# Kernel optimization log

Hardware: AMD Instinct MI355X
Metric: run time of the kernel (lower is better)

## Reference

```python
import jax, jax.numpy as jnp
import numpy as np
import math

V, TB, C, H, L = 50257, 1024, 1024, 16, 8
B, T = 2, 1024
D = C // H


def setup_inputs() -> dict:
    key = jax.random.key(0)
    ks = jax.random.split(key, 16)
    s = 0.02
    n = lambda k, shp: (jax.random.normal(k, shp, jnp.float32) * s)
    inp = {
        "idx": jax.random.randint(ks[0], (B, T), 0, V),
        "tok_emb": n(ks[1], (V, C)),
        "pos_emb": n(ks[2], (1, TB, C)),
        # per-layer stacked params (torch Linear convention: W is [out, in])
        "Wq": n(ks[3], (L, C, C)), "bq": jnp.zeros((L, C)),
        "Wk": n(ks[4], (L, C, C)), "bk": jnp.zeros((L, C)),
        "Wv": n(ks[5], (L, C, C)), "bv": jnp.zeros((L, C)),
        "Wp": n(ks[6], (L, C, C)), "bp": jnp.zeros((L, C)),
        "ln1_w": jnp.ones((L, C)), "ln1_b": jnp.zeros((L, C)),
        "ln2_w": jnp.ones((L, C)), "ln2_b": jnp.zeros((L, C)),
        "W1": n(ks[7], (L, 4 * C, C)), "b1": jnp.zeros((L, 4 * C)),
        "W2": n(ks[8], (L, C, 4 * C)), "b2": jnp.zeros((L, C)),
        "lnf_w": jnp.ones((C,)), "lnf_b": jnp.zeros((C,)),
        "head_w": n(ks[9], (V, C)),
    }
    return inp


def _layer_norm(x, w, b, eps=1e-5):
    mu = x.mean(-1, keepdims=True)
    var = x.var(-1, keepdims=True)
    return (x - mu) * jax.lax.rsqrt(var + eps) * w + b


def _gpt_forward(idx, tok_emb, pos_emb, Wq, bq, Wk, bk, Wv, bv, Wp, bp,
                 ln1_w, ln1_b, ln2_w, ln2_b, W1, b1, W2, b2, lnf_w, lnf_b, head_w):
    b, t = idx.shape
    x = tok_emb[idx] + pos_emb[:, :t, :]  # [B, T, C]; drop = identity (eval)
    causal = jnp.tril(jnp.ones((t, t), dtype=bool))  # [T, T]
    scale = 1.0 / math.sqrt(D)

    def block(x, p):
        (wq, bq_, wk, bk_, wv, bv_, wp, bp_, l1w, l1b, l2w, l2b, w1, b1_, w2, b2_) = p
        h = _layer_norm(x, l1w, l1b)
        q = (h @ wq.T + bq_).reshape(b, t, H, D).transpose(0, 2, 1, 3)  # [B,H,T,D]
        k = (h @ wk.T + bk_).reshape(b, t, H, D).transpose(0, 2, 1, 3)
        v = (h @ wv.T + bv_).reshape(b, t, H, D).transpose(0, 2, 1, 3)
        att = jnp.einsum("bhqd,bhkd->bhqk", q, k) * scale
        att = jnp.where(causal, att, -jnp.inf)
        att = jax.nn.softmax(att, axis=-1)
        y = jnp.einsum("bhqk,bhkd->bhqd", att, v)
        y = y.transpose(0, 2, 1, 3).reshape(b, t, C)
        x = x + (y @ wp.T + bp_)
        h2 = _layer_norm(x, l2w, l2b)
        m = jax.nn.gelu(h2 @ w1.T + b1_, approximate=False)  # torch nn.GELU (erf)
        x = x + (m @ w2.T + b2_)
        return x, None

    params = (Wq, bq, Wk, bk, Wv, bv, Wp, bp, ln1_w, ln1_b, ln2_w, ln2_b, W1, b1, W2, b2)
    x, _ = jax.lax.scan(block, x, params)
    x = _layer_norm(x, lnf_w, lnf_b)
    logits = x @ head_w.T  # [B, T, V]
    return logits


def reference(idx, tok_emb, pos_emb, Wq, bq, Wk, bk, Wv, bv, Wp, bp,
              ln1_w, ln1_b, ln2_w, ln2_b, W1, b1, W2, b2, lnf_w, lnf_b, head_w):
    return _gpt_forward(idx, tok_emb, pos_emb, Wq, bq, Wk, bk, Wv, bv, Wp, bp,
                        ln1_w, ln1_b, ln2_w, ln2_b, W1, b1, W2, b2, lnf_w, lnf_b, head_w)
```

## Files before the change

kernel.cpp:

```cpp
#include <hip/hip_runtime.h>
#include <math.h>

#define V_ 50257
#define C_ 1024
#define H_ 16
#define L_ 8
#define B_ 2
#define T_ 1024
#define BT_ 2048
#define CC_ (C_*C_)
#define QLD_ 3072

typedef unsigned short ushort_t;
using bf16x8 = __attribute__((ext_vector_type(8))) short;
using f32x4  = __attribute__((ext_vector_type(4))) float;

#define AS1 __attribute__((address_space(1)))
#define AS3 __attribute__((address_space(3)))
#define VMCNT0() asm volatile("s_waitcnt vmcnt(0)" ::: "memory")
#define LGKM0()  asm volatile("s_waitcnt lgkmcnt(0)" ::: "memory")
#define RBAR()   asm volatile("s_barrier" ::: "memory")

__device__ __forceinline__ ushort_t f2bf(float f){
  union { float f; unsigned u; } a; a.f = f;
  unsigned r = a.u + 0x7fffu + ((a.u >> 16) & 1u);
  return (ushort_t)(r >> 16);
}

__device__ __forceinline__ unsigned cvtpk_bf16(float a, float b){
  unsigned r;
  asm("v_cvt_pk_bf16_f32 %0, %1, %2" : "=v"(r) : "v"(a), "v"(b));
  return r;
}

__device__ __forceinline__ float wave_sum(float v){
  #pragma unroll
  for(int o=32;o>0;o>>=1) v += __shfl_down(v,o,64);
  return v;
}

__global__ __launch_bounds__(256) void cvt_blk(const float* __restrict__ s, ushort_t* __restrict__ d,
    long inner4, int nblk, long dstStride4){
  long total = inner4 * nblk;
  for(long i = (long)blockIdx.x*256 + threadIdx.x; i < total; i += (long)gridDim.x*256){
    long blk = i / inner4, r = i - blk*inner4;
    float4 v = ((const float4*)s)[i];
    ushort4 o; o.x=f2bf(v.x); o.y=f2bf(v.y); o.z=f2bf(v.z); o.w=f2bf(v.w);
    ((ushort4*)d)[blk*dstStride4 + r] = o;
  }
}

__global__ __launch_bounds__(256) void pack_qkv_bias(const float* __restrict__ bq,
    const float* __restrict__ bk, const float* __restrict__ bv, float* __restrict__ dst){
  int i = blockIdx.x*256 + threadIdx.x;
  int l = i / QLD_, c = i - l*QLD_;
  float v;
  if(c < C_)            v = bq[l*C_ + c];
  else if(c < 2*C_)     v = bk[l*C_ + c - C_];
  else                  v = bv[l*C_ + c - 2*C_];
  dst[i] = v;
}

__global__ __launch_bounds__(256) void embed_kernel(const int* __restrict__ idx,
    const float* __restrict__ tok, const float* __restrict__ pos, float* __restrict__ x){
  int i = blockIdx.x*256 + threadIdx.x;
  int c = i & (C_-1); int bt = i >> 10; int t = bt & (T_-1);
  x[i] = tok[(size_t)idx[bt]*C_ + c] + pos[t*C_ + c];
}

__global__ __launch_bounds__(256) void ln_kernel(const float* in, const float* __restrict__ w,
    const float* __restrict__ b, float* outF, ushort_t* outB){
  int row = blockIdx.x;
  const float* xr = in + (size_t)row*C_;
  float vals[4]; float sum=0.f, sq=0.f;
  #pragma unroll
  for(int l=0;l<4;l++){ float v = xr[threadIdx.x + l*256]; vals[l]=v; sum+=v; sq+=v*v; }
  __shared__ float r1[4], r2[4];
  float s1 = wave_sum(sum), s2 = wave_sum(sq);
  int wid = threadIdx.x>>6, lane = threadIdx.x&63;
  if(lane==0){ r1[wid]=s1; r2[wid]=s2; }
  __syncthreads();
  float tot  = r1[0]+r1[1]+r1[2]+r1[3];
  float tot2 = r2[0]+r2[1]+r2[2]+r2[3];
  float mu  = tot * (1.f/C_);
  float var = tot2 * (1.f/C_) - mu*mu;
  float inv = rsqrtf(var + 1e-5f);
  #pragma unroll
  for(int l=0;l<4;l++){
    int c = threadIdx.x + l*256;
    float v = (vals[l]-mu)*inv*w[c] + b[c];
    if(outB) outB[(size_t)row*C_ + c] = f2bf(v);
    else     outF[(size_t)row*C_ + c] = v;
  }
}

template<int BN>
__global__ __launch_bounds__(256) void gemm_mfma(
    const ushort_t* __restrict__ A, const ushort_t* __restrict__ W,
    const float* __restrict__ bias, const float* resid,
    float* outF, ushort_t* outB,
    int M, int N, int K, int act, int nt, int qs)
{
  constexpr int BM = 128;
  constexpr int NSB = BN/16;
  constexpr int NBF = BN/32;
  __shared__ __align__(16) short sA[3][8*512];
  __shared__ __align__(16) short sB[3][NSB*512];
  const int tid  = threadIdx.x;
  const int lane = tid & 63, wid = tid >> 6;
  const int wr = wid >> 1, wc = wid & 1;
  const int nwg = gridDim.x * gridDim.y;
  const int lid = blockIdx.x + gridDim.x * blockIdx.y;
  const int swz = (lid & 7) * (nwg >> 3) + (lid >> 3);
  const int m0 = (swz % gridDim.x) * BM, n0 = (swz / gridDim.x) * BN;
  const int r16 = lane & 15, kq = lane >> 4;

  auto stage = [&](int buf, int k0){
    #pragma unroll
    for(int s2=0; s2<2; ++s2){
      int s = wid*2 + s2;
      const ushort_t* g = A + (size_t)(m0 + s*16 + r16)*K + k0 + kq*8;
      __builtin_amdgcn_global_load_lds((const AS1 void*)g,
          (AS3 void*)&sA[buf][s*512], 16, 0, 0);
    }
    #pragma unroll
    for(int s2=0; s2<NSB/4; ++s2){
      int s = wid*(NSB/4) + s2;
      int gn = n0 + s*16 + r16; if(gn >= N) gn = N-1;
      const ushort_t* g = W + (size_t)gn*K + k0 + kq*8;
      __builtin_amdgcn_global_load_lds((const AS1 void*)g,
          (AS3 void*)&sB[buf][s*512], 16, 0, 0);
    }
  };

  f32x4 acc[4][NBF];
  #pragma unroll
  for(int i=0;i<4;i++)
    #pragma unroll
    for(int j=0;j<NBF;j++) acc[i][j] = (f32x4){0.f,0.f,0.f,0.f};

  const int NT = K >> 5;
  stage(0, 0); stage(1, 32); stage(2, 64);

  int cur = 0;
  for(int t=0; t<NT; ++t){
    if(t+2 < NT){
      if constexpr(BN==128) asm volatile("s_waitcnt vmcnt(8)" ::: "memory");
      else                  asm volatile("s_waitcnt vmcnt(6)" ::: "memory");
    } else if(t+1 < NT){
      if constexpr(BN==128) asm volatile("s_waitcnt vmcnt(4)" ::: "memory");
      else                  asm volatile("s_waitcnt vmcnt(3)" ::: "memory");
    } else {
      VMCNT0();
    }
    RBAR();
    bf16x8 af[4], bfr[NBF];
    #pragma unroll
    for(int m=0;m<4;m++) af[m] = *(const bf16x8*)&sA[cur][(wr*4+m)*512 + lane*8];
    #pragma unroll
    for(int n=0;n<NBF;n++) bfr[n] = *(const bf16x8*)&sB[cur][(wc*NBF+n)*512 + lane*8];
    LGKM0();
    RBAR();
    if(t+3 < NT) stage(cur, (t+3)*32);
    #pragma unroll
    for(int m=0;m<4;m++)
      #pragma unroll
      for(int n=0;n<NBF;n++)
        acc[m][n] = __builtin_amdgcn_mfma_f32_16x16x32_bf16(af[m], bfr[n], acc[m][n], 0, 0, 0);
    cur = (cur==2) ? 0 : cur+1;
  }

  const int colb = n0 + wc*(BN/2);
  #pragma unroll
  for(int m=0;m<4;m++){
    int rowb = m0 + wr*64 + m*16 + kq*4;
    #pragma unroll
    for(int n=0;n<NBF;n++){
      int col = colb + n*16 + r16;
      if(col >= N) continue;
      float bv = bias ? bias[col] : 0.f;
      #pragma unroll
      for(int i=0;i<4;i++){
        int row = rowb + i;
        float v = acc[m][n][i] + bv;
        if(qs && col < C_) v *= 0.125f;
        if(act) v = 0.5f*v*(1.f + erff(v*0.70710678118654752f));
        if(resid) v += resid[(size_t)row*N + col];
        if(outB) outB[(size_t)row*N + col] = f2bf(v);
        else if(nt) __builtin_nontemporal_store(v, &outF[(size_t)row*N + col]);
        else outF[(size_t)row*N + col] = v;
      }
    }
  }
}

__global__ __launch_bounds__(256) void flash_kernel(const ushort_t* __restrict__ qkv,
    ushort_t* __restrict__ y){
  const int tid = threadIdx.x, lane = tid & 63, wid = tid >> 6;
  const int r16 = lane & 15, kq = lane >> 4;
  const int lid = blockIdx.x + 16*blockIdx.y;
  const int swz = (lid & 7)*64 + (lid >> 3);
  const int qt = swz & 15, bh = swz >> 4;
  const int b = bh >> 4, h = bh & 15;
  const int q0 = qt*64, qw0 = q0 + wid*16;
  const int qa = qw0 + r16;

  __shared__ __align__(16) short Kt[2][8][512];
  __shared__ __align__(16) short VT[2][64][68];
  __shared__ __align__(16) short Pl[4][16][68];
  __shared__ __align__(16) short Ol[4][16][68];

  const size_t rowQ = (size_t)(b*T_ + qa)*QLD_ + h*64 + kq*8;
  bf16x8 qf0 = *(const bf16x8*)(qkv + rowQ);
  bf16x8 qf1 = *(const bf16x8*)(qkv + rowQ + 32);

  auto stageK = [&](int buf, int jt){
    #pragma unroll
    for(int s2=0;s2<2;s2++){
      int s = wid*2 + s2;
      const ushort_t* g = qkv + (size_t)(b*T_ + jt*64 + (s>>1)*16 + r16)*QLD_
                          + C_ + h*64 + (s&1)*32 + kq*8;
      __builtin_amdgcn_global_load_lds((const AS1 void*)g,
          (AS3 void*)&Kt[buf][s][lane*8], 16, 0, 0);
    }
  };

  f32x4 acc[4];
  #pragma unroll
  for(int t=0;t<4;t++) acc[t] = (f32x4){0.f,0.f,0.f,0.f};
  float m_r = -INFINITY, l_r = 0.f;

  {
    stageK(0, 0);
    const ushort_t* vg = qkv + (size_t)(b*T_ + lane)*QLD_ + 2*C_ + h*64;
    bf16x8 va = *(const bf16x8*)(vg + wid*8);
    bf16x8 vb = *(const bf16x8*)(vg + 32 + wid*8);
    VMCNT0();
    #pragma unroll
    for(int j=0;j<8;j++){ VT[0][wid*8+j][lane]=va[j]; VT[0][32+wid*8+j][lane]=vb[j]; }
    __syncthreads();
  }

  const int njt = qt + 1;
  for(int jt=0; jt<njt; ++jt){
    const int cur = jt & 1;
    const bool more = (jt+1) < njt;
    bf16x8 vr0, vr1;
    if(more){
      stageK(cur^1, jt+1);
      const ushort_t* vg = qkv + (size_t)(b*T_ + (jt+1)*64 + lane)*QLD_ + 2*C_ + h*64;
      vr0 = *(const bf16x8*)(vg + wid*8);
      vr1 = *(const bf16x8*)(vg + 32 + wid*8);
    }

    f32x4 st[4];
    __builtin_amdgcn_s_setprio(1);
    #pragma unroll
    for(int kr=0;kr<4;kr++){
      st[kr] = (f32x4){0.f,0.f,0.f,0.f};
      st[kr] = __builtin_amdgcn_mfma_f32_16x16x32_bf16(*(const bf16x8*)&Kt[cur][kr*2+0][lane*8], qf0, st[kr], 0,0,0);
      st[kr] = __builtin_amdgcn_mfma_f32_16x16x32_bf16(*(const bf16x8*)&Kt[cur][kr*2+1][lane*8], qf1, st[kr], 0,0,0);
    }
    __builtin_amdgcn_s_setprio(0);

    float vals[16];
    if(jt == njt-1){
      #pragma unroll
      for(int kr=0;kr<4;kr++)
        #pragma unroll
        for(int i=0;i<4;i++){
          int ka = jt*64 + kr*16 + 4*kq + i;
          vals[kr*4+i] = (ka <= qa) ? st[kr][i] : -INFINITY;
        }
    } else {
      #pragma unroll
      for(int kr=0;kr<4;kr++)
        #pragma unroll
        for(int i=0;i<4;i++) vals[kr*4+i] = st[kr][i];
    }
    float t8[8];
    #pragma unroll
    for(int i=0;i<8;i++) t8[i] = fmaxf(vals[i], vals[i+8]);
    float t4a = fmaxf(t8[0],t8[4]), t4b = fmaxf(t8[1],t8[5]);
    float t4c = fmaxf(t8[2],t8[6]), t4d = fmaxf(t8[3],t8[7]);
    float pmax = fmaxf(fmaxf(t4a,t4b), fmaxf(t4c,t4d));
    pmax = fmaxf(pmax, __shfl_xor(pmax, 16, 64));
    pmax = fmaxf(pmax, __shfl_xor(pmax, 32, 64));

    if(!__all(pmax - m_r <= 8.f)){
      float mnew = fmaxf(m_r, pmax);
      float alpha = __expf(m_r - mnew);
      l_r *= alpha;
      #pragma unroll
      for(int t=0;t<4;t++)
        #pragma unroll
        for(int j=0;j<4;j++) acc[t][j] *= alpha;
      m_r = mnew;
    }

    float ps = 0.f;
    #pragma unroll
    for(int kr=0;kr<4;kr++){
      float p0 = __expf(vals[kr*4+0]-m_r), p1 = __expf(vals[kr*4+1]-m_r);
      float p2 = __expf(vals[kr*4+2]-m_r), p3 = __expf(vals[kr*4+3]-m_r);
      ps += (p0+p1)+(p2+p3);
      *(unsigned*)&Pl[wid][r16][kr*16 + 4*kq]     = cvtpk_bf16(p0, p1);
      *(unsigned*)&Pl[wid][r16][kr*16 + 4*kq + 2] = cvtpk_bf16(p2, p3);
    }
    ps += __shfl_xor(ps, 16, 64);
    ps += __shfl_xor(ps, 32, 64);
    l_r += ps;

    union { bf16x8 v8; uint2 u2[2]; } pf, vf;
    __builtin_amdgcn_s_setprio(1);
    #pragma unroll
    for(int ks2=0; ks2<2; ks2++){
      pf.u2[0] = *(const uint2*)&Pl[wid][r16][ks2*32 + kq*8];
      pf.u2[1] = *(const uint2*)&Pl[wid][r16][ks2*32 + kq*8 + 4];
      #pragma unroll
      for(int db=0; db<4; db++){
        vf.u2[0] = *(const uint2*)&VT[cur][16*db + r16][ks2*32 + kq*8];
        vf.u2[1] = *(const uint2*)&VT[cur][16*db + r16][ks2*32 + kq*8 + 4];
        acc[db] = __builtin_amdgcn_mfma_f32_16x16x32_bf16(vf.v8, pf.v8, acc[db], 0,0,0);
      }
    }
    __builtin_amdgcn_s_setprio(0);

    if(more){
      VMCNT0();
      #pragma unroll
      for(int j=0;j<8;j++){ VT[cur^1][wid*8+j][lane]=vr0[j]; VT[cur^1][32+wid*8+j][lane]=vr1[j]; }
    }
    __syncthreads();
  }

  float linv = 1.f / l_r;
  #pragma unroll
  for(int db=0; db<4; db++)
    #pragma unroll
    for(int i=0;i<4;i++)
      Ol[wid][r16][16*db + 4*kq + i] = (short)f2bf(acc[db][i]*linv);
  int q = lane >> 2, c0 = (lane & 3)*16;
  const short* src = &Ol[wid][q][c0];
  uint2 a0 = *(const uint2*)(src+0), a1 = *(const uint2*)(src+4);
  uint2 a2 = *(const uint2*)(src+8), a3 = *(const uint2*)(src+12);
  ushort_t* dst = y + (size_t)(b*T_ + qw0 + q)*C_ + h*64 + c0;
  uint4 w0 = {a0.x, a0.y, a1.x, a1.y}, w1 = {a2.x, a2.y, a3.x, a3.y};
  *(uint4*)(dst+0) = w0;
  *(uint4*)(dst+8) = w1;
}

__global__ __launch_bounds__(256) void gemm_nt(const float* __restrict__ A, const float* __restrict__ W,
    const float* __restrict__ bias, const float* resid, float* Cm,
    int M, int N, int K, int act){
  __shared__ float As[16][68];
  __shared__ float Bs[16][68];
  int m0 = blockIdx.y*64, n0 = blockIdx.x*64;
  int tid = threadIdx.x;
  int tx = tid & 15, ty = tid >> 4;
  float acc[4][4] = {};
  for(int k0=0;k0<K;k0+=16){
    #pragma unroll
    for(int l=0;l<4;l++){
      int li = tid + l*256;
      int r = li >> 4, c = li & 15;
      int gm = m0 + r, gn = n0 + r, gk = k0 + c;
      As[c][r] = (gm<M) ? A[(size_t)gm*K + gk] : 0.f;
      Bs[c][r] = (gn<N) ? W[(size_t)gn*K + gk] : 0.f;
    }
    __syncthreads();
    #pragma unroll
    for(int k=0;k<16;k++){
      float4 av = *(const float4*)&As[k][ty*4];
      float4 bv = *(const float4*)&Bs[k][tx*4];
      float a[4] = {av.x, av.y, av.z, av.w};
      float b4[4] = {bv.x, bv.y, bv.z, bv.w};
      #pragma unroll
      for(int i=0;i<4;i++)
        #pragma unroll
        for(int j=0;j<4;j++)
          acc[i][j] = fmaf(a[i], b4[j], acc[i][j]);
    }
    __syncthreads();
  }
  #pragma unroll
  for(int i=0;i<4;i++){
    int m = m0 + ty*4 + i; if(m>=M) continue;
    #pragma unroll
    for(int j=0;j<4;j++){
      int n = n0 + tx*4 + j; if(n>=N) continue;
      float v = acc[i][j];
      if(bias) v += bias[n];
      if(act)  v = 0.5f*v*(1.f + erff(v*0.70710678118654752f));
      if(resid) v += resid[(size_t)m*N + n];
      Cm[(size_t)m*N + n] = v;
    }
  }
}

extern "C" void kernel_launch(void* const* d_in, const int* in_sizes, int n_in,
                              void* d_out, int out_size, void* d_ws, size_t ws_size,
                              hipStream_t stream) {
  const int*   idx  = (const int*)  d_in[0];
  const float* tok  = (const float*)d_in[1];
  const float* pos  = (const float*)d_in[2];
  const float* Wq   = (const float*)d_in[3];
  const float* bq   = (const float*)d_in[4];
  const float* Wk   = (const float*)d_in[5];
  const float* bk   = (const float*)d_in[6];
  const float* Wv   = (const float*)d_in[7];
  const float* bv   = (const float*)d_in[8];
  const float* Wp   = (const float*)d_in[9];
  const float* bp   = (const float*)d_in[10];
  const float* ln1w = (const float*)d_in[11];
  const float* ln1b = (const float*)d_in[12];
  const float* ln2w = (const float*)d_in[13];
  const float* ln2b = (const float*)d_in[14];
  const float* W1   = (const float*)d_in[15];
  const float* b1   = (const float*)d_in[16];
  const float* W2   = (const float*)d_in[17];
  const float* b2   = (const float*)d_in[18];
  const float* lnfw = (const float*)d_in[19];
  const float* lnfb = (const float*)d_in[20];
  const float* headw= (const float*)d_in[21];

  float* out = (float*)d_out;
  ushort_t* qkvb = (ushort_t*)(out);
  ushort_t* hb   = (ushort_t*)(out + 3145728);
  ushort_t* yb   = (ushort_t*)(out + 4194304);
  ushort_t* mb   = (ushort_t*)(out + 5242880);
  ushort_t* wqkv = (ushort_t*)(out + 9437184);
  ushort_t* wpb  = (ushort_t*)(out + 22020096);
  ushort_t* w1b  = (ushort_t*)(out + 26214400);
  ushort_t* w2b  = (ushort_t*)(out + 42991616);
  float*    bqkv = out + 59768832;
  float*    x    = (float*)d_ws;
  ushort_t* xb   = (ushort_t*)((float*)d_ws + 2097152);
  ushort_t* whb  = (ushort_t*)((float*)d_ws + 3145728);
  const bool big = ws_size >= (size_t)28877312 * 4;

  cvt_blk<<<2048,256,0,stream>>>(Wq, wqkv,          CC_/4, L_, 3*CC_/4);
  cvt_blk<<<2048,256,0,stream>>>(Wk, wqkv + CC_,    CC_/4, L_, 3*CC_/4);
  cvt_blk<<<2048,256,0,stream>>>(Wv, wqkv + 2*CC_,  CC_/4, L_, 3*CC_/4);
  cvt_blk<<<2048,256,0,stream>>>(Wp, wpb,  (long)L_*CC_/4,   1, (long)L_*CC_/4);
  cvt_blk<<<2048,256,0,stream>>>(W1, w1b,  (long)L_*CC_,     1, (long)L_*CC_);
  cvt_blk<<<2048,256,0,stream>>>(W2, w2b,  (long)L_*CC_,     1, (long)L_*CC_);
  if(big) cvt_blk<<<2048,256,0,stream>>>(headw, whb, (long)V_*C_/4, 1, (long)V_*C_/4);
  pack_qkv_bias<<<L_*QLD_/256,256,0,stream>>>(bq, bk, bv, bqkv);

  embed_kernel<<<BT_*C_/256, 256, 0, stream>>>(idx, tok, pos, x);

  for(int l=0;l<L_;l++){
    ln_kernel<<<BT_,256,0,stream>>>(x, ln1w + l*C_, ln1b + l*C_, nullptr, hb);
    gemm_mfma<128><<<dim3(BT_/128, QLD_/128),256,0,stream>>>(hb, wqkv + (size_t)l*3*CC_,
        bqkv + l*QLD_, nullptr, nullptr, qkvb, BT_, QLD_, C_, 0, 0, 1);
    flash_kernel<<<dim3(T_/64, B_*H_),256,0,stream>>>(qkvb, yb);
    gemm_mfma<64><<<dim3(BT_/128, C_/64),256,0,stream>>>(yb, wpb + (size_t)l*CC_,
        bp + l*C_, x, x, nullptr, BT_, C_, C_, 0, 0, 0);
    ln_kernel<<<BT_,256,0,stream>>>(x, ln2w + l*C_, ln2b + l*C_, nullptr, hb);
    gemm_mfma<128><<<dim3(BT_/128, 4*C_/128),256,0,stream>>>(hb, w1b + (size_t)l*4*CC_,
        b1 + (size_t)l*4*C_, nullptr, nullptr, mb, BT_, 4*C_, C_, 1, 0, 0);
    gemm_mfma<64><<<dim3(BT_/128, C_/64),256,0,stream>>>(mb, w2b + (size_t)l*4*CC_,
        b2 + l*C_, x, x, nullptr, BT_, C_, 4*C_, 0, 0, 0);
  }

  if(big){
    ln_kernel<<<BT_,256,0,stream>>>(x, lnfw, lnfb, nullptr, xb);
    gemm_mfma<128><<<dim3(BT_/128, (V_+127)/128),256,0,stream>>>(xb, whb,
        nullptr, nullptr, out, nullptr, BT_, V_, C_, 0, 1, 0);
  } else {
    ln_kernel<<<BT_,256,0,stream>>>(x, lnfw, lnfb, x, nullptr);
    gemm_nt<<<dim3((V_+63)/64, BT_/64),256,0,stream>>>(x, headw, nullptr, nullptr, out,
                                                       BT_, V_, C_, 0);
  }
}
```

Before: 2.719 ms.

## Add 256x128 triple-buffered GEMM for LM head and widen flash LDS padding

Adds a dedicated LM-head GEMM kernel with a 256x128 output tile, three-stage LDS buffering via direct global-to-LDS loads, and a swizzled block order. Each wave now computes 8x4 MFMA tiles, which raises arithmetic intensity and overlaps loads two steps ahead, aiming to cut the cost of the large vocab projection that dominates runtime. It also changes the flash-attention LDS row padding from 68 to 72 shorts to alter bank-conflict behaviour. The cost is higher register and LDS pressure, which may limit occupancy.

```diff
diff --git a/kernel.cpp b/kernel.cpp
--- a/kernel.cpp
+++ b/kernel.cpp
@@ -194,6 +194,84 @@
   }
 }
 
+__global__ __launch_bounds__(256, 2) void gemm_big(
+    const ushort_t* __restrict__ A, const ushort_t* __restrict__ W,
+    float* __restrict__ outF, int M, int N, int K)
+{
+  __shared__ __align__(16) short sA[3][16*512];
+  __shared__ __align__(16) short sB[3][8*512];
+  const int tid  = threadIdx.x;
+  const int lane = tid & 63, wid = tid >> 6;
+  const int wr = wid >> 1, wc = wid & 1;
+  const int nwg = gridDim.x * gridDim.y;
+  const int lid = blockIdx.x + gridDim.x * blockIdx.y;
+  const int swz = (lid & 7) * (nwg >> 3) + (lid >> 3);
+  const int m0 = (swz % gridDim.x) * 256, n0 = (swz / gridDim.x) * 128;
+  const int r16 = lane & 15, kq = lane >> 4;
+
+  auto stage = [&](int buf, int k0){
+    #pragma unroll
+    for(int s2=0; s2<4; ++s2){
+      int s = wid*4 + s2;
+      const ushort_t* g = A + (size_t)(m0 + s*16 + r16)*K + k0 + kq*8;
+      __builtin_amdgcn_global_load_lds((const AS1 void*)g,
+          (AS3 void*)&sA[buf][s*512], 16, 0, 0);
+    }
+    #pragma unroll
+    for(int s2=0; s2<2; ++s2){
+      int s = wid*2 + s2;
+      int gn = n0 + s*16 + r16; if(gn >= N) gn = N-1;
+      const ushort_t* g = W + (size_t)gn*K + k0 + kq*8;
+      __builtin_amdgcn_global_load_lds((const AS1 void*)g,
+          (AS3 void*)&sB[buf][s*512], 16, 0, 0);
+    }
+  };
+
+  f32x4 acc[8][4];
+  #pragma unroll
+  for(int i=0;i<8;i++)
+    #pragma unroll
+    for(int j=0;j<4;j++) acc[i][j] = (f32x4){0.f,0.f,0.f,0.f};
+
+  const int NT = K >> 5;
+  stage(0, 0); stage(1, 32); stage(2, 64);
+
+  int cur = 0;
+  for(int t=0; t<NT; ++t){
+    if(t+2 < NT)      asm volatile("s_waitcnt vmcnt(12)" ::: "memory");
+    else if(t+1 < NT) asm volatile("s_waitcnt vmcnt(6)"  ::: "memory");
+    else              VMCNT0();
+    RBAR();
+    bf16x8 af[8], bfr[4];
+    #pragma unroll
+    for(int m=0;m<8;m++) af[m] = *(const bf16x8*)&sA[cur][(wr*8+m)*512 + lane*8];
+    #pragma unroll
+    for(int n=0;n<4;n++) bfr[n] = *(const bf16x8*)&sB[cur][(wc*4+n)*512 + lane*8];
+    LGKM0();
+    RBAR();
+    if(t+3 < NT) stage(cur, (t+3)*32);
+    #pragma unroll
+    for(int m=0;m<8;m++)
+      #pragma unroll
+      for(int n=0;n<4;n++)
+        acc[m][n] = __builtin_amdgcn_mfma_f32_16x16x32_bf16(af[m], bfr[n], acc[m][n], 0, 0, 0);
+    cur = (cur==2) ? 0 : cur+1;
+  }
+
+  #pragma unroll
+  for(int m=0;m<8;m++){
+    int rowb = m0 + wr*128 + m*16 + kq*4;
+    #pragma unroll
+    for(int n=0;n<4;n++){
+      int col = n0 + wc*64 + n*16 + r16;
+      if(col >= N) continue;
+      #pragma unroll
+      for(int i=0;i<4;i++)
+        __builtin_nontemporal_store(acc[m][n][i], &outF[(size_t)(rowb+i)*N + col]);
+    }
+  }
+}
+
 __global__ __launch_bounds__(256) void flash_kernel(const ushort_t* __restrict__ qkv,
     ushort_t* __restrict__ y){
   const int tid = threadIdx.x, lane = tid & 63, wid = tid >> 6;
@@ -206,9 +284,9 @@
   const int qa = qw0 + r16;
 
   __shared__ __align__(16) short Kt[2][8][512];
-  __shared__ __align__(16) short VT[2][64][68];
-  __shared__ __align__(16) short Pl[4][16][68];
-  __shared__ __align__(16) short Ol[4][16][68];
+  __shared__ __align__(16) short VT[2][64][72];
+  __shared__ __align__(16) short Pl[4][16][72];
+  __shared__ __align__(16) short Ol[4][16][72];
 
   const size_t rowQ = (size_t)(b*T_ + qa)*QLD_ + h*64 + kq*8;
   bf16x8 qf0 = *(const bf16x8*)(qkv + rowQ);
@@ -466,8 +544,7 @@
 
   if(big){
     ln_kernel<<<BT_,256,0,stream>>>(x, lnfw, lnfb, nullptr, xb);
-    gemm_mfma<128><<<dim3(BT_/128, (V_+127)/128),256,0,stream>>>(xb, whb,
-        nullptr, nullptr, out, nullptr, BT_, V_, C_, 0, 1, 0);
+    gemm_big<<<dim3(BT_/256, (V_+127)/128),256,0,stream>>>(xb, whb, out, BT_, V_, C_);
   } else {
     ln_kernel<<<BT_,256,0,stream>>>(x, lnfw, lnfb, x, nullptr);
     gemm_nt<<<dim3((V_+63)/64, BT_/64),256,0,stream>>>(x, headw, nullptr, nullptr, out,
```

Result: no change. 2.746 ms (+1.0%).
